# Optimization experiments

Measured on AMD Instinct MI355X. Metric: run time of the kernel, lower is better.

Reference implementation:

```python
import jax, jax.numpy as jnp
import numpy as np

TOP_K = 4  # router top-k


def setup_inputs() -> dict:
    key = jax.random.key(0)
    ks = jax.random.split(key, 8)
    B, S, D, E, H, HS = 2, 2048, 2048, 16, 1024, 4096
    scaled = lambda k, shape, fan: (jax.random.normal(k, shape, jnp.float32) * (fan ** -0.5))
    return {
        "x": jax.random.normal(ks[0], (B, S, D), jnp.float32),
        "w_router": scaled(ks[1], (D, E), D),
        # per-expert SwiGLU MLP weights
        "we1": scaled(ks[2], (E, D, H), D),
        "we3": scaled(ks[3], (E, D, H), D),
        "we2": scaled(ks[4], (E, H, D), H),
        # shared SwiGLU MLP weights
        "ws1": scaled(ks[5], (D, HS), D),
        "ws3": scaled(ks[6], (D, HS), D),
        "ws2": scaled(ks[7], (HS, D), HS),
    }


def reference(x, w_router, we1, we3, we2, ws1, ws3, ws2):
    B, S, D = x.shape
    T = B * S
    E = w_router.shape[1]
    xt = x.reshape(T, D)

    # ---- router: softmax over experts, top-k, renormalize top-k weights ----
    probs = jax.nn.softmax(xt @ w_router, axis=-1)           # [T, E]
    top_w, top_i = jax.lax.top_k(probs, TOP_K)               # [T, K]
    top_w = top_w / jnp.sum(top_w, axis=-1, keepdims=True)
    # dense combine weights [T, E] (zero for non-selected experts)
    cw = jnp.zeros((T, E), xt.dtype).at[jnp.arange(T)[:, None], top_i].add(top_w)

    # ---- experts: per-expert SwiGLU, combine with routing weights ----
    g = jax.nn.silu(jnp.einsum("td,edh->teh", xt, we1)) * jnp.einsum("td,edh->teh", xt, we3)
    g = g * cw[:, :, None]                                   # fold combine weight in
    moe_out = jnp.einsum("teh,ehd->td", g, we2)              # [T, D]

    # ---- shared MLP (SwiGLU) and blend ----
    shared = (jax.nn.silu(xt @ ws1) * (xt @ ws3)) @ ws2      # [T, D]
    k = TOP_K
    out = shared / (k + 1) + moe_out * (k / (k + 1))
    return out.reshape(B, S, D)
```

## Files before the change

kernel.cpp:

```cpp
#include <hip/hip_runtime.h>
#include <stdint.h>

#define TTOK  4096
#define DDIM  2048
#define NEXP  16
#define HDIM  1024
#define HSDIM 4096
#define CAPR  18432

typedef __bf16 bf16x8 __attribute__((ext_vector_type(8)));
typedef float  f32x4  __attribute__((ext_vector_type(4)));

__device__ __forceinline__ unsigned short f2b(float f) {
  union { float f; unsigned int i; } v; v.f = f;
  unsigned int r = (v.i + 0x7fffu + ((v.i >> 16) & 1u)) >> 16;
  return (unsigned short)r;
}
__device__ __forceinline__ float b2f(unsigned short u) {
  union { unsigned int i; float f; } v; v.i = ((unsigned int)u) << 16; return v.f;
}
__device__ __forceinline__ float silu_f(float x) { return x / (1.f + __expf(-x)); }

__device__ __forceinline__ void gload16(const void* g, void* l) {
  __builtin_amdgcn_global_load_lds(
      (const __attribute__((address_space(1))) unsigned int*)(uintptr_t)g,
      (__attribute__((address_space(3))) unsigned int*)(uintptr_t)l,
      16, 0, 0);
}

__device__ __forceinline__ int xcd_swz(int bid, int nwg) {
  int q = nwg >> 3, r = nwg & 7;
  int xcd = bid & 7, off = bid >> 3;
  return (xcd < r ? xcd * (q + 1) : r * (q + 1) + (xcd - r) * q) + off;
}

__device__ __forceinline__ void tile_map(int wg, int MB, int NB, int& mb, int& nb) {
  int st = wg >> 5;
  int in = wg & 31;
  int sm = MB >> 2;
  int stm = st % sm;
  int stn = st / sm;
  mb = stm * 4 + (in >> 3);
  nb = stn * 8 + (in & 7);
}

__global__ void cvt_bf16_kernel(const float* __restrict__ in, unsigned short* __restrict__ out, int n8) {
  int i = blockIdx.x * 256 + threadIdx.x;
  if (i >= n8) return;
  const float4* p = (const float4*)in + (size_t)i * 2;
  float4 a = p[0], b = p[1];
  uint4 o;
  o.x = (unsigned)f2b(a.x) | ((unsigned)f2b(a.y) << 16);
  o.y = (unsigned)f2b(a.z) | ((unsigned)f2b(a.w) << 16);
  o.z = (unsigned)f2b(b.x) | ((unsigned)f2b(b.y) << 16);
  o.w = (unsigned)f2b(b.z) | ((unsigned)f2b(b.w) << 16);
  ((uint4*)out)[i] = o;
}

__global__ __launch_bounds__(256) void transpose_f2b(const float* __restrict__ in,
                                                     unsigned short* __restrict__ out, int R, int C) {
  __shared__ unsigned short t[64][68];
  size_t zo = (size_t)blockIdx.z * (size_t)R * C;
  int c0 = blockIdx.x * 64, r0 = blockIdx.y * 64;
  int tid = threadIdx.x;
#pragma unroll
  for (int p = 0; p < 4; ++p) {
    int id = p * 256 + tid;
    int r = id >> 4;
    int c4 = (id & 15) * 4;
    float4 v = *(const float4*)&in[zo + (size_t)(r0 + r) * C + c0 + c4];
    ushort4 w = { f2b(v.x), f2b(v.y), f2b(v.z), f2b(v.w) };
    *(ushort4*)&t[r][c4] = w;
  }
  __syncthreads();
#pragma unroll
  for (int p = 0; p < 2; ++p) {
    int id = p * 256 + tid;
    int c = id >> 3;
    int r8 = (id & 7) * 8;
    unsigned p0 = (unsigned)t[r8 + 0][c] | ((unsigned)t[r8 + 1][c] << 16);
    unsigned p1 = (unsigned)t[r8 + 2][c] | ((unsigned)t[r8 + 3][c] << 16);
    unsigned p2 = (unsigned)t[r8 + 4][c] | ((unsigned)t[r8 + 5][c] << 16);
    unsigned p3 = (unsigned)t[r8 + 6][c] | ((unsigned)t[r8 + 7][c] << 16);
    uint4 o = { p0, p1, p2, p3 };
    *(uint4*)&out[zo + (size_t)(c0 + c) * R + r0 + r8] = o;
  }
}

__global__ __launch_bounds__(256) void router_kernel(const float* __restrict__ x, const float* __restrict__ wr,
                                                     float* __restrict__ topw, int* __restrict__ topi) {
  int tok = blockIdx.x * 4 + (threadIdx.x >> 6);
  int lane = threadIdx.x & 63;
  const float* xr = x + (size_t)tok * DDIM;
  float acc[NEXP];
#pragma unroll
  for (int e = 0; e < NEXP; ++e) acc[e] = 0.f;
  for (int it = 0; it < DDIM / 64; ++it) {
    int d = it * 64 + lane;
    float xv = xr[d];
    const float4* w4 = (const float4*)(wr + (size_t)d * NEXP);
    float4 w0 = w4[0], w1 = w4[1], w2 = w4[2], w3 = w4[3];
    acc[0] += xv * w0.x; acc[1] += xv * w0.y; acc[2] += xv * w0.z; acc[3] += xv * w0.w;
    acc[4] += xv * w1.x; acc[5] += xv * w1.y; acc[6] += xv * w1.z; acc[7] += xv * w1.w;
    acc[8] += xv * w2.x; acc[9] += xv * w2.y; acc[10] += xv * w2.z; acc[11] += xv * w2.w;
    acc[12] += xv * w3.x; acc[13] += xv * w3.y; acc[14] += xv * w3.z; acc[15] += xv * w3.w;
  }
#pragma unroll
  for (int e = 0; e < NEXP; ++e) {
#pragma unroll
    for (int off = 32; off > 0; off >>= 1) acc[e] += __shfl_xor(acc[e], off);
  }
  unsigned used = 0u;
  float lv[4]; int si[4];
#pragma unroll
  for (int k = 0; k < 4; ++k) {
    float best = -3.4e38f; int bi = 0;
    for (int e = 0; e < NEXP; ++e) {
      if (!((used >> e) & 1u) && acc[e] > best) { best = acc[e]; bi = e; }
    }
    used |= 1u << bi; lv[k] = best; si[k] = bi;
  }
  if (lane == 0) {
    float m = lv[0], s = 0.f, w[4];
#pragma unroll
    for (int k = 0; k < 4; ++k) { w[k] = __expf(lv[k] - m); s += w[k]; }
    float inv = 1.f / s;
#pragma unroll
    for (int k = 0; k < 4; ++k) { topw[tok * 4 + k] = w[k] * inv; topi[tok * 4 + k] = si[k]; }
  }
}

__global__ void zero_kernel(int* b) { if (threadIdx.x < 64) b[threadIdx.x] = 0; }

__global__ void count_kernel(const int* __restrict__ topi, int* counts, int n) {
  int i = blockIdx.x * 256 + threadIdx.x;
  if (i < n) atomicAdd(&counts[topi[i]], 1);
}

__global__ void offsets_kernel(const int* counts, int* eoff) {
  if (threadIdx.x == 0 && blockIdx.x == 0) {
    int o = 0;
    for (int e = 0; e < NEXP; ++e) { eoff[e] = o; o += (counts[e] + 127) & ~127; }
    eoff[NEXP] = o;
  }
}

__global__ void prefill_kernel(int* gtok, float* gwt, int cap) {
  int i = blockIdx.x * 256 + threadIdx.x;
  if (i < cap) { gtok[i] = 0; gwt[i] = 0.f; }
}

__global__ void scatter_kernel(const int* __restrict__ topi, const float* __restrict__ topw,
                               const int* __restrict__ eoff, int* cursors,
                               int* gtok, float* gwt, int* posmap, int n) {
  int i = blockIdx.x * 256 + threadIdx.x;
  if (i >= n) return;
  int e = topi[i];
  int pos = eoff[e] + atomicAdd(&cursors[e], 1);
  gtok[pos] = i >> 2;
  gwt[pos] = topw[i] * 0.8f;
  posmap[i] = pos;
}

__global__ __launch_bounds__(256) void combine_kernel(const unsigned short* __restrict__ ecout,
                                                      const int* __restrict__ posmap,
                                                      float* __restrict__ out, int n8) {
  int i = blockIdx.x * 256 + threadIdx.x;
  if (i >= n8) return;
  int t = i >> 8;
  int c = i & 255;
  int4 pv = *(const int4*)&posmap[t * 4];
  float s[8];
  float4 o0 = ((const float4*)out)[(size_t)i * 2];
  float4 o1 = ((const float4*)out)[(size_t)i * 2 + 1];
  s[0]=o0.x; s[1]=o0.y; s[2]=o0.z; s[3]=o0.w; s[4]=o1.x; s[5]=o1.y; s[6]=o1.z; s[7]=o1.w;
  int pos[4] = {pv.x, pv.y, pv.z, pv.w};
#pragma unroll
  for (int k = 0; k < 4; ++k) {
    uint4 v = ((const uint4*)(ecout + (size_t)pos[k] * DDIM))[c];
    unsigned* pw = (unsigned*)&v;
#pragma unroll
    for (int w = 0; w < 4; ++w) {
      s[w * 2]     += b2f((unsigned short)(pw[w] & 0xffffu));
      s[w * 2 + 1] += b2f((unsigned short)(pw[w] >> 16));
    }
  }
  float4 r0 = {s[0], s[1], s[2], s[3]}, r1 = {s[4], s[5], s[6], s[7]};
  ((float4*)out)[(size_t)i * 2] = r0;
  ((float4*)out)[(size_t)i * 2 + 1] = r1;
}

template <int MODE>
__global__ __launch_bounds__(512) void gemm_dual(const unsigned short* __restrict__ A,
                                                 const unsigned short* __restrict__ W1,
                                                 const unsigned short* __restrict__ W3,
                                                 unsigned short* __restrict__ G,
                                                 int N, int K, int MB,
                                                 const int* __restrict__ gtok,
                                                 const float* __restrict__ gwt,
                                                 const int* __restrict__ eoff) {
  __shared__ unsigned short sA[128 * 64];
  __shared__ unsigned short s1[128 * 64];
  __shared__ unsigned short s3[128 * 64];
  __shared__ int sIdx[128];

  int nwg = gridDim.x;
  int wg = xcd_swz(blockIdx.x, nwg);
  int mb, nb;
  tile_map(wg, MB, nwg / MB, mb, nb);
  int m0 = mb * 128;
  int n0 = nb * 128;

  const unsigned short* W1e = W1;
  const unsigned short* W3e = W3;
  if constexpr (MODE == 2) {
    if (m0 >= eoff[NEXP]) return;
    int e = 0;
    while (m0 >= eoff[e + 1]) ++e;
    size_t wofs = (size_t)e * N * K;
    W1e += wofs; W3e += wofs;
  }

  int tid = threadIdx.x, lane = tid & 63, wv = tid >> 6;
  if constexpr (MODE == 2) {
    if (tid < 128) sIdx[tid] = gtok[m0 + tid];
    __syncthreads();
  }

  int wm = wv >> 2, wn = wv & 3;
  f32x4 ac1[4][2], ac3[4][2];
#pragma unroll
  for (int mi = 0; mi < 4; ++mi)
#pragma unroll
    for (int ni = 0; ni < 2; ++ni) { ac1[mi][ni] = (f32x4){0,0,0,0}; ac3[mi][ni] = (f32x4){0,0,0,0}; }

  for (int kt = 0; kt < K; kt += 64) {
#pragma unroll
    for (int c = 0; c < 2; ++c) {
      int bofs = (wv * 2 + c) * 1024 + lane * 16;
      int row = bofs >> 7;
      int sch = ((bofs >> 4) & 7) ^ (row & 7);
      int ar;
      if constexpr (MODE == 2) ar = sIdx[row]; else ar = m0 + row;
      gload16(A   + (size_t)ar * K        + kt + sch * 8, &sA[(wv * 2 + c) * 512]);
      gload16(W1e + (size_t)(n0 + row) * K + kt + sch * 8, &s1[(wv * 2 + c) * 512]);
      gload16(W3e + (size_t)(n0 + row) * K + kt + sch * 8, &s3[(wv * 2 + c) * 512]);
    }
    __syncthreads();
#pragma unroll
    for (int kk = 0; kk < 2; ++kk) {
      bf16x8 af[4], b1[2], b3[2];
#pragma unroll
      for (int mi = 0; mi < 4; ++mi) {
        int row = wm * 64 + mi * 16 + (lane & 15);
        int ch = (kk * 4 + (lane >> 4)) ^ (row & 7);
        af[mi] = *(const bf16x8*)&sA[row * 64 + ch * 8];
      }
#pragma unroll
      for (int ni = 0; ni < 2; ++ni) {
        int row = wn * 32 + ni * 16 + (lane & 15);
        int ch = (kk * 4 + (lane >> 4)) ^ (row & 7);
        b1[ni] = *(const bf16x8*)&s1[row * 64 + ch * 8];
        b3[ni] = *(const bf16x8*)&s3[row * 64 + ch * 8];
      }
#pragma unroll
      for (int mi = 0; mi < 4; ++mi)
#pragma unroll
        for (int ni = 0; ni < 2; ++ni) {
          ac1[mi][ni] = __builtin_amdgcn_mfma_f32_16x16x32_bf16(af[mi], b1[ni], ac1[mi][ni], 0, 0, 0);
          ac3[mi][ni] = __builtin_amdgcn_mfma_f32_16x16x32_bf16(af[mi], b3[ni], ac3[mi][ni], 0, 0, 0);
        }
    }
    __syncthreads();
  }

#pragma unroll
  for (int mi = 0; mi < 4; ++mi)
#pragma unroll
    for (int ni = 0; ni < 2; ++ni) {
      int cc = n0 + wn * 32 + ni * 16 + (lane & 15);
#pragma unroll
      for (int j = 0; j < 4; ++j) {
        int rr = m0 + wm * 64 + mi * 16 + ((lane >> 4) << 2) + j;
        float sc;
        if constexpr (MODE == 2) sc = gwt[rr]; else sc = 1.f;
        float g = silu_f(ac1[mi][ni][j]) * ac3[mi][ni][j] * sc;
        G[(size_t)rr * N + cc] = f2b(g);
      }
    }
}

template <int MODE>
__global__ __launch_bounds__(512) void gemm_bt8(const unsigned short* __restrict__ A,
                                                const unsigned short* __restrict__ Bt,
                                                unsigned short* __restrict__ Cbf,
                                                float* __restrict__ Cf,
                                                int N, int K, int MB,
                                                const int* __restrict__ eoff,
                                                float scale) {
  __shared__ unsigned short sA[128 * 64];
  __shared__ unsigned short sB[256 * 64];

  int nwg = gridDim.x;
  int wg = xcd_swz(blockIdx.x, nwg);
  int mb, nb;
  tile_map(wg, MB, nwg / MB, mb, nb);
  int m0 = mb * 128;
  int n0 = nb * 256;

  const unsigned short* Bte = Bt;
  if constexpr (MODE == 4) {
    if (m0 >= eoff[NEXP]) return;
    int e = 0;
    while (m0 >= eoff[e + 1]) ++e;
    Bte = Bt + (size_t)e * N * K;
  }
  int tid = threadIdx.x, lane = tid & 63, wv = tid >> 6;
  int wm = wv >> 2, wn = wv & 3;
  f32x4 acc[4][4];
#pragma unroll
  for (int mi = 0; mi < 4; ++mi)
#pragma unroll
    for (int ni = 0; ni < 4; ++ni) acc[mi][ni] = (f32x4){0.f, 0.f, 0.f, 0.f};

  for (int kt = 0; kt < K; kt += 64) {
#pragma unroll
    for (int c = 0; c < 2; ++c) {
      int bofs = (wv * 2 + c) * 1024 + lane * 16;
      int row = bofs >> 7;
      int sch = ((bofs >> 4) & 7) ^ (row & 7);
      gload16(A + (size_t)(m0 + row) * K + kt + sch * 8, &sA[(wv * 2 + c) * 512]);
    }
#pragma unroll
    for (int c = 0; c < 4; ++c) {
      int bofs = (wv * 4 + c) * 1024 + lane * 16;
      int row = bofs >> 7;
      int sch = ((bofs >> 4) & 7) ^ (row & 7);
      gload16(Bte + (size_t)(n0 + row) * K + kt + sch * 8, &sB[(wv * 4 + c) * 512]);
    }
    __syncthreads();
#pragma unroll
    for (int kk = 0; kk < 2; ++kk) {
      bf16x8 af[4], bfv[4];
#pragma unroll
      for (int mi = 0; mi < 4; ++mi) {
        int row = wm * 64 + mi * 16 + (lane & 15);
        int ch = (kk * 4 + (lane >> 4)) ^ (row & 7);
        af[mi] = *(const bf16x8*)&sA[row * 64 + ch * 8];
      }
#pragma unroll
      for (int ni = 0; ni < 4; ++ni) {
        int row = wn * 64 + ni * 16 + (lane & 15);
        int ch = (kk * 4 + (lane >> 4)) ^ (row & 7);
        bfv[ni] = *(const bf16x8*)&sB[row * 64 + ch * 8];
      }
#pragma unroll
      for (int mi = 0; mi < 4; ++mi)
#pragma unroll
        for (int ni = 0; ni < 4; ++ni)
          acc[mi][ni] = __builtin_amdgcn_mfma_f32_16x16x32_bf16(af[mi], bfv[ni], acc[mi][ni], 0, 0, 0);
    }
    __syncthreads();
  }

#pragma unroll
  for (int mi = 0; mi < 4; ++mi)
#pragma unroll
    for (int ni = 0; ni < 4; ++ni) {
      int cc = n0 + wn * 64 + ni * 16 + (lane & 15);
#pragma unroll
      for (int j = 0; j < 4; ++j) {
        int rr = m0 + wm * 64 + mi * 16 + ((lane >> 4) << 2) + j;
        float v = acc[mi][ni][j];
        if constexpr (MODE == 1) Cf[(size_t)rr * N + cc] = v * scale;
        else Cbf[(size_t)rr * N + cc] = f2b(v);
      }
    }
}

extern "C" void kernel_launch(void* const* d_in, const int* in_sizes, int n_in,
                              void* d_out, int out_size, void* d_ws, size_t ws_size,
                              hipStream_t stream) {
  const float* x   = (const float*)d_in[0];
  const float* wr  = (const float*)d_in[1];
  const float* we1 = (const float*)d_in[2];
  const float* we3 = (const float*)d_in[3];
  const float* we2 = (const float*)d_in[4];
  const float* ws1 = (const float*)d_in[5];
  const float* ws3 = (const float*)d_in[6];
  const float* ws2 = (const float*)d_in[7];
  float* out = (float*)d_out;

  char* p = (char*)d_ws;
  auto take = [&](size_t bytes) { char* r = p; p += (bytes + 255) & ~(size_t)255; return r; };
  unsigned short* xbf   = (unsigned short*)take((size_t)TTOK * DDIM * 2);
  unsigned short* ehg   = (unsigned short*)take((size_t)CAPR * HDIM * 2);
  unsigned short* gsh   = (unsigned short*)take((size_t)TTOK * HSDIM * 2);
  unsigned short* ecout = (unsigned short*)take((size_t)CAPR * DDIM * 2);
  unsigned short* twArena = (unsigned short*)take((size_t)NEXP * HDIM * DDIM * 2);
  float* topw = (float*)take((size_t)TTOK * 4 * 4);
  int*   topi = (int*)take((size_t)TTOK * 4 * 4);
  int*   gtok = (int*)take((size_t)CAPR * 4);
  float* gwt  = (float*)take((size_t)CAPR * 4);
  int*   posmap = (int*)take((size_t)TTOK * 4 * 4);
  int*   ibuf = (int*)take(256);
  if ((size_t)(p - (char*)d_ws) > ws_size) return;

  unsigned short* twA = twArena;
  unsigned short* twB = twArena + (size_t)8 * DDIM * HDIM;
  unsigned short* we3t = gsh;

  int* counts  = ibuf;
  int* cursors = ibuf + 16;
  int* eoff    = ibuf + 32;

  cvt_bf16_kernel<<<TTOK * DDIM / 8 / 256, 256, 0, stream>>>(x, xbf, TTOK * DDIM / 8);
  router_kernel<<<TTOK / 4, 256, 0, stream>>>(x, wr, topw, topi);
  zero_kernel<<<1, 64, 0, stream>>>(ibuf);
  count_kernel<<<TTOK * 4 / 256, 256, 0, stream>>>(topi, counts, TTOK * 4);
  offsets_kernel<<<1, 64, 0, stream>>>(counts, eoff);
  prefill_kernel<<<CAPR / 256, 256, 0, stream>>>(gtok, gwt, CAPR);
  scatter_kernel<<<TTOK * 4 / 256, 256, 0, stream>>>(topi, topw, eoff, cursors, gtok, gwt, posmap, TTOK * 4);

  transpose_f2b<<<dim3(HSDIM / 64, DDIM / 64, 1), 256, 0, stream>>>(ws1, twA, DDIM, HSDIM);
  transpose_f2b<<<dim3(HSDIM / 64, DDIM / 64, 1), 256, 0, stream>>>(ws3, twB, DDIM, HSDIM);
  gemm_dual<0><<<(TTOK / 128) * (HSDIM / 128), 512, 0, stream>>>(xbf, twA, twB, gsh, HSDIM, DDIM,
                                                                 TTOK / 128, nullptr, nullptr, nullptr);
  transpose_f2b<<<dim3(DDIM / 64, HSDIM / 64, 1), 256, 0, stream>>>(ws2, twA, HSDIM, DDIM);
  gemm_bt8<1><<<(TTOK / 128) * (DDIM / 256), 512, 0, stream>>>(gsh, twA, nullptr, out, DDIM, HSDIM,
                                                               TTOK / 128, nullptr, 0.2f);

  transpose_f2b<<<dim3(HDIM / 64, DDIM / 64, NEXP), 256, 0, stream>>>(we1, twArena, DDIM, HDIM);
  transpose_f2b<<<dim3(HDIM / 64, DDIM / 64, NEXP), 256, 0, stream>>>(we3, we3t, DDIM, HDIM);
  gemm_dual<2><<<(CAPR / 128) * (HDIM / 128), 512, 0, stream>>>(xbf, twArena, we3t, ehg, HDIM, DDIM,
                                                                CAPR / 128, gtok, gwt, eoff);
  transpose_f2b<<<dim3(DDIM / 64, HDIM / 64, NEXP), 256, 0, stream>>>(we2, twArena, HDIM, DDIM);
  gemm_bt8<4><<<(CAPR / 128) * (DDIM / 256), 512, 0, stream>>>(ehg, twArena, ecout, nullptr, DDIM, HDIM,
                                                               CAPR / 128, eoff, 0.f);

  combine_kernel<<<TTOK * DDIM / 8 / 256, 256, 0, stream>>>(ecout, posmap, out, TTOK * DDIM / 8);
}
```

Before: 792.5 us.

## Fuse fp32 weight transpose and bf16 conversion into GEMM LDS staging

Removes the separate transpose_f2b passes over all shared and expert weights. The GEMMs now read fp32 weights directly in their native [K,N] layout, convert them to bf16 in registers and write them transposed and swizzled into LDS. This drops the extra write and re-read of transposed bf16 weight copies. In exchange, each tile re-reads fp32 weights (twice the bytes) from global memory, and every M-block does this redundantly. The asynchronous global_load_lds path for weights is replaced with synchronous register loads plus LDS stores.

```diff
diff --git a/kernel.cpp b/kernel.cpp
--- a/kernel.cpp
+++ b/kernel.cpp
@@ -9,6 +9,7 @@
 #define CAPR  18432
 
 typedef __bf16 bf16x8 __attribute__((ext_vector_type(8)));
+typedef __bf16 bf16x4 __attribute__((ext_vector_type(4)));
 typedef float  f32x4  __attribute__((ext_vector_type(4)));
 
 __device__ __forceinline__ unsigned short f2b(float f) {
@@ -42,6 +43,27 @@
   int stn = st / sm;
   mb = stm * 4 + (in >> 3);
   nb = stn * 8 + (in & 7);
+}
+
+__device__ __forceinline__ void stage_w_f32(const float* __restrict__ Wsrc, int N,
+                                            unsigned short* lds, int tid) {
+  const int kq = (tid & 15) * 4;
+  const int nq = (tid >> 4) * 4;
+  const float* p = Wsrc + (size_t)kq * N + nq;
+  float a[4][4] __attribute__((aligned(16)));
+  *(float4*)a[0] = *(const float4*)p;
+  *(float4*)a[1] = *(const float4*)(p + (size_t)N);
+  *(float4*)a[2] = *(const float4*)(p + 2 * (size_t)N);
+  *(float4*)a[3] = *(const float4*)(p + 3 * (size_t)N);
+  const int kch = kq >> 3;
+  const int ksub = (kq & 4) * 2;
+#pragma unroll
+  for (int j = 0; j < 4; ++j) {
+    int row = nq + j;
+    int byte = row * 128 + ((kch ^ (row & 7)) << 4) + ksub;
+    bf16x4 w = { (__bf16)a[0][j], (__bf16)a[1][j], (__bf16)a[2][j], (__bf16)a[3][j] };
+    *(bf16x4*)((char*)lds + byte) = w;
+  }
 }
 
 __global__ void cvt_bf16_kernel(const float* __restrict__ in, unsigned short* __restrict__ out, int n8) {
@@ -55,36 +77,6 @@
   o.z = (unsigned)f2b(b.x) | ((unsigned)f2b(b.y) << 16);
   o.w = (unsigned)f2b(b.z) | ((unsigned)f2b(b.w) << 16);
   ((uint4*)out)[i] = o;
-}
-
-__global__ __launch_bounds__(256) void transpose_f2b(const float* __restrict__ in,
-                                                     unsigned short* __restrict__ out, int R, int C) {
-  __shared__ unsigned short t[64][68];
-  size_t zo = (size_t)blockIdx.z * (size_t)R * C;
-  int c0 = blockIdx.x * 64, r0 = blockIdx.y * 64;
-  int tid = threadIdx.x;
-#pragma unroll
-  for (int p = 0; p < 4; ++p) {
-    int id = p * 256 + tid;
-    int r = id >> 4;
-    int c4 = (id & 15) * 4;
-    float4 v = *(const float4*)&in[zo + (size_t)(r0 + r) * C + c0 + c4];
-    ushort4 w = { f2b(v.x), f2b(v.y), f2b(v.z), f2b(v.w) };
-    *(ushort4*)&t[r][c4] = w;
-  }
-  __syncthreads();
-#pragma unroll
-  for (int p = 0; p < 2; ++p) {
-    int id = p * 256 + tid;
-    int c = id >> 3;
-    int r8 = (id & 7) * 8;
-    unsigned p0 = (unsigned)t[r8 + 0][c] | ((unsigned)t[r8 + 1][c] << 16);
-    unsigned p1 = (unsigned)t[r8 + 2][c] | ((unsigned)t[r8 + 3][c] << 16);
-    unsigned p2 = (unsigned)t[r8 + 4][c] | ((unsigned)t[r8 + 5][c] << 16);
-    unsigned p3 = (unsigned)t[r8 + 6][c] | ((unsigned)t[r8 + 7][c] << 16);
-    uint4 o = { p0, p1, p2, p3 };
-    *(uint4*)&out[zo + (size_t)(c0 + c) * R + r0 + r8] = o;
-  }
 }
 
 __global__ __launch_bounds__(256) void router_kernel(const float* __restrict__ x, const float* __restrict__ wr,
@@ -192,8 +184,8 @@
 
 template <int MODE>
 __global__ __launch_bounds__(512) void gemm_dual(const unsigned short* __restrict__ A,
-                                                 const unsigned short* __restrict__ W1,
-                                                 const unsigned short* __restrict__ W3,
+                                                 const float* __restrict__ W1,
+                                                 const float* __restrict__ W3,
                                                  unsigned short* __restrict__ G,
                                                  int N, int K, int MB,
                                                  const int* __restrict__ gtok,
@@ -211,8 +203,8 @@
   int m0 = mb * 128;
   int n0 = nb * 128;
 
-  const unsigned short* W1e = W1;
-  const unsigned short* W3e = W3;
+  const float* W1e = W1;
+  const float* W3e = W3;
   if constexpr (MODE == 2) {
     if (m0 >= eoff[NEXP]) return;
     int e = 0;
@@ -242,10 +234,10 @@
       int sch = ((bofs >> 4) & 7) ^ (row & 7);
       int ar;
       if constexpr (MODE == 2) ar = sIdx[row]; else ar = m0 + row;
-      gload16(A   + (size_t)ar * K        + kt + sch * 8, &sA[(wv * 2 + c) * 512]);
-      gload16(W1e + (size_t)(n0 + row) * K + kt + sch * 8, &s1[(wv * 2 + c) * 512]);
-      gload16(W3e + (size_t)(n0 + row) * K + kt + sch * 8, &s3[(wv * 2 + c) * 512]);
-    }
+      gload16(A + (size_t)ar * K + kt + sch * 8, &sA[(wv * 2 + c) * 512]);
+    }
+    stage_w_f32(W1e + (size_t)kt * N + n0, N, s1, tid);
+    stage_w_f32(W3e + (size_t)kt * N + n0, N, s3, tid);
     __syncthreads();
 #pragma unroll
     for (int kk = 0; kk < 2; ++kk) {
@@ -292,7 +284,7 @@
 
 template <int MODE>
 __global__ __launch_bounds__(512) void gemm_bt8(const unsigned short* __restrict__ A,
-                                                const unsigned short* __restrict__ Bt,
+                                                const float* __restrict__ Bf,
                                                 unsigned short* __restrict__ Cbf,
                                                 float* __restrict__ Cf,
                                                 int N, int K, int MB,
@@ -308,12 +300,12 @@
   int m0 = mb * 128;
   int n0 = nb * 256;
 
-  const unsigned short* Bte = Bt;
+  const float* Bte = Bf;
   if constexpr (MODE == 4) {
     if (m0 >= eoff[NEXP]) return;
     int e = 0;
     while (m0 >= eoff[e + 1]) ++e;
-    Bte = Bt + (size_t)e * N * K;
+    Bte = Bf + (size_t)e * N * K;
   }
   int tid = threadIdx.x, lane = tid & 63, wv = tid >> 6;
   int wm = wv >> 2, wn = wv & 3;
@@ -331,13 +323,8 @@
       int sch = ((bofs >> 4) & 7) ^ (row & 7);
       gload16(A + (size_t)(m0 + row) * K + kt + sch * 8, &sA[(wv * 2 + c) * 512]);
     }
-#pragma unroll
-    for (int c = 0; c < 4; ++c) {
-      int bofs = (wv * 4 + c) * 1024 + lane * 16;
-      int row = bofs >> 7;
-      int sch = ((bofs >> 4) & 7) ^ (row & 7);
-      gload16(Bte + (size_t)(n0 + row) * K + kt + sch * 8, &sB[(wv * 4 + c) * 512]);
-    }
+    stage_w_f32(Bte + (size_t)kt * N + n0,       N, sB,            tid);
+    stage_w_f32(Bte + (size_t)kt * N + n0 + 128, N, sB + 128 * 64, tid);
     __syncthreads();
 #pragma unroll
     for (int kk = 0; kk < 2; ++kk) {
@@ -397,7 +384,6 @@
   unsigned short* ehg   = (unsigned short*)take((size_t)CAPR * HDIM * 2);
   unsigned short* gsh   = (unsigned short*)take((size_t)TTOK * HSDIM * 2);
   unsigned short* ecout = (unsigned short*)take((size_t)CAPR * DDIM * 2);
-  unsigned short* twArena = (unsigned short*)take((size_t)NEXP * HDIM * DDIM * 2);
   float* topw = (float*)take((size_t)TTOK * 4 * 4);
   int*   topi = (int*)take((size_t)TTOK * 4 * 4);
   int*   gtok = (int*)take((size_t)CAPR * 4);
@@ -406,10 +392,6 @@
   int*   ibuf = (int*)take(256);
   if ((size_t)(p - (char*)d_ws) > ws_size) return;
 
-  unsigned short* twA = twArena;
-  unsigned short* twB = twArena + (size_t)8 * DDIM * HDIM;
-  unsigned short* we3t = gsh;
-
   int* counts  = ibuf;
   int* cursors = ibuf + 16;
   int* eoff    = ibuf + 32;
@@ -422,20 +404,14 @@
   prefill_kernel<<<CAPR / 256, 256, 0, stream>>>(gtok, gwt, CAPR);
   scatter_kernel<<<TTOK * 4 / 256, 256, 0, stream>>>(topi, topw, eoff, cursors, gtok, gwt, posmap, TTOK * 4);
 
-  transpose_f2b<<<dim3(HSDIM / 64, DDIM / 64, 1), 256, 0, stream>>>(ws1, twA, DDIM, HSDIM);
-  transpose_f2b<<<dim3(HSDIM / 64, DDIM / 64, 1), 256, 0, stream>>>(ws3, twB, DDIM, HSDIM);
-  gemm_dual<0><<<(TTOK / 128) * (HSDIM / 128), 512, 0, stream>>>(xbf, twA, twB, gsh, HSDIM, DDIM,
+  gemm_dual<0><<<(TTOK / 128) * (HSDIM / 128), 512, 0, stream>>>(xbf, ws1, ws3, gsh, HSDIM, DDIM,
                                                                  TTOK / 128, nullptr, nullptr, nullptr);
-  transpose_f2b<<<dim3(DDIM / 64, HSDIM / 64, 1), 256, 0, stream>>>(ws2, twA, HSDIM, DDIM);
-  gemm_bt8<1><<<(TTOK / 128) * (DDIM / 256), 512, 0, stream>>>(gsh, twA, nullptr, out, DDIM, HSDIM,
+  gemm_bt8<1><<<(TTOK / 128) * (DDIM / 256), 512, 0, stream>>>(gsh, ws2, nullptr, out, DDIM, HSDIM,
                                                                TTOK / 128, nullptr, 0.2f);
 
-  transpose_f2b<<<dim3(HDIM / 64, DDIM / 64, NEXP), 256, 0, stream>>>(we1, twArena, DDIM, HDIM);
-  transpose_f2b<<<dim3(HDIM / 64, DDIM / 64, NEXP), 256, 0, stream>>>(we3, we3t, DDIM, HDIM);
-  gemm_dual<2><<<(CAPR / 128) * (HDIM / 128), 512, 0, stream>>>(xbf, twArena, we3t, ehg, HDIM, DDIM,
+  gemm_dual<2><<<(CAPR / 128) * (HDIM / 128), 512, 0, stream>>>(xbf, we1, we3, ehg, HDIM, DDIM,
                                                                 CAPR / 128, gtok, gwt, eoff);
-  transpose_f2b<<<dim3(DDIM / 64, HDIM / 64, NEXP), 256, 0, stream>>>(we2, twArena, HDIM, DDIM);
-  gemm_bt8<4><<<(CAPR / 128) * (DDIM / 256), 512, 0, stream>>>(ehg, twArena, ecout, nullptr, DDIM, HDIM,
+  gemm_bt8<4><<<(CAPR / 128) * (DDIM / 256), 512, 0, stream>>>(ehg, we2, ecout, nullptr, DDIM, HDIM,
                                                                CAPR / 128, eoff, 0.f);
 
   combine_kernel<<<TTOK * DDIM / 8 / 256, 256, 0, stream>>>(ecout, posmap, out, TTOK * DDIM / 8);
```

New measurement: 1.419 ms. 79.1% more time.
